# Optimization experiments

Hardware: AMD Instinct MI355X
Metric: run time of the kernel (lower is better)

The kernel has to match this reference:

```python
import jax, jax.numpy as jnp
import numpy as np

N_ENTITIES = 500000
N_RELATIONS = 200
EMBED_DIM = 128
RELATION_DIM = 128  # must equal EMBED_DIM for the reshape in calculate_score
BATCH = 16384
KG_L2_LAMBDA = 1e-5


def _xavier_uniform(key, shape):
    fan_in, fan_out = shape[0], shape[1]
    limit = float(np.sqrt(6.0 / (fan_in + fan_out)))
    return jax.random.uniform(key, shape, jnp.float32, -limit, limit)


def setup_inputs() -> dict:
    key = jax.random.key(0)
    k1, k2, k3, k4, k5, k6 = jax.random.split(key, 6)
    entity_embed = _xavier_uniform(k1, (N_ENTITIES, EMBED_DIM))
    relation_embed = _xavier_uniform(k2, (N_RELATIONS, RELATION_DIM * EMBED_DIM))
    h = jax.random.randint(k3, (BATCH,), 0, N_ENTITIES, dtype=jnp.int64)
    r = jax.random.randint(k4, (BATCH,), 0, N_RELATIONS, dtype=jnp.int64)
    pos_t = jax.random.randint(k5, (BATCH,), 0, N_ENTITIES, dtype=jnp.int64)
    neg_t = jax.random.randint(k6, (BATCH,), 0, N_ENTITIES, dtype=jnp.int64)
    return {"h": h, "r": r, "pos_t": pos_t, "neg_t": neg_t,
            "entity_embed": entity_embed, "relation_embed": relation_embed}


def _l2_loss_mean(x):
    # mean over batch of sum(x^2, dim=1) / 2
    return jnp.mean(jnp.sum(x * x, axis=1) / 2.0)


def _score(h_e, t_e, r_mat):
    # r_mat: (B, relation_dim, embed_dim); tr = r @ t : (B, embed_dim)
    tr = jnp.einsum('bde,be->bd', r_mat, t_e)
    return -jnp.sum(h_e * tr, axis=-1)  # (B,)


def reference(h, r, pos_t, neg_t, entity_embed, relation_embed):
    r_embed = relation_embed[r]                     # (B, R*D)
    head_embed = entity_embed[h]                    # (B, D)
    tail_pos_embed = entity_embed[pos_t]            # (B, D)
    tail_neg_embed = entity_embed[neg_t]            # (B, D)
    r_mat = r_embed.reshape(-1, RELATION_DIM, EMBED_DIM)
    pos_score = _score(head_embed, tail_pos_embed, r_mat)
    neg_score = _score(head_embed, tail_neg_embed, r_mat)
    triplet_loss = jnp.mean(-jax.nn.log_sigmoid(neg_score - pos_score))
    l2_loss = (_l2_loss_mean(head_embed) + _l2_loss_mean(r_embed)
               + _l2_loss_mean(tail_pos_embed) + _l2_loss_mean(tail_neg_embed))
    return triplet_loss + KG_L2_LAMBDA * l2_loss
```

## Files before the change

kernel.cpp:

```cpp
#include <hip/hip_runtime.h>
#include <math.h>

#define BATCH 16384
#define EDIM 128
#define RD (EDIM * EDIM)
#define NREL 200
#define SPLIT 4
#define NBLK (NREL * SPLIT)
#define NTHR 512
#define QUARTER (BATCH / SPLIT)
#define NJ (QUARTER / NTHR)
#define EBW 4
#define LISTCAP 256


__device__ __forceinline__ int load_idx(const void* p, int b, int is64) {
    if (is64) return (int)((const long long*)p)[b];
    return ((const int*)p)[b];
}

__global__ __launch_bounds__(NTHR, 4) void rescal_kernel(
    const void* __restrict__ hI, const void* __restrict__ rI,
    const void* __restrict__ pI, const void* __restrict__ nI,
    const float* __restrict__ ent, const float* __restrict__ rel,
    float* __restrict__ csum) {
    const int t = threadIdx.x;
    const int bid0 = blockIdx.x;
    const int xcd = bid0 & 7;
    const int slot = bid0 >> 3;
    const int rid = xcd + 8 * (slot >> 2);
    const int qtr = slot & 3;
    const int lane = t & 63;
    const int wave = t >> 6;
    const int c2 = lane * 2;

    __shared__ __attribute__((aligned(16))) float Rl[RD];
    __shared__ unsigned short list[LISTCAP];
    __shared__ unsigned int wtj[NJ][8];
    __shared__ unsigned int um8[8];
    __shared__ float rsq[8], wsum[8];

    unsigned int o = 0u;
    if (t < 256) {
        o = ((const unsigned int*)hI)[2 * t + 1] | ((const unsigned int*)rI)[2 * t + 1] |
            ((const unsigned int*)pI)[2 * t + 1] | ((const unsigned int*)nI)[2 * t + 1];
    }
#pragma unroll
    for (int off = 32; off; off >>= 1) o |= __shfl_xor(o, off, 64);
    if (lane == 0) um8[wave] = o;
    __syncthreads();
    const int is64 = ((um8[0] | um8[1] | um8[2] | um8[3] |
                       um8[4] | um8[5] | um8[6] | um8[7]) == 0u) ? 1 : 0;

    const float* Rg = rel + (size_t)rid * RD;
    float r2p = 0.f;
#pragma unroll
    for (int it = 0; it < 8; ++it) {
        const int idx = it * (NTHR * 4) + t * 4;
        const float4 v = *(const float4*)(Rg + idx);
        *(float4*)&Rl[idx] = v;
        r2p = fmaf(v.x, v.x, fmaf(v.y, v.y, fmaf(v.z, v.z, fmaf(v.w, v.w, r2p))));
    }
#pragma unroll
    for (int off = 32; off; off >>= 1) r2p += __shfl_xor(r2p, off, 64);
    if (lane == 0) rsq[wave] = r2p;

    const int qbase = qtr * QUARTER;
    unsigned long long bal[NJ];
#pragma unroll
    for (int j = 0; j < NJ; ++j) {
        const int rr = load_idx(rI, qbase + j * NTHR + t, is64);
        bal[j] = __ballot(rr == rid);
        if (lane == 0) wtj[j][wave] = (unsigned int)__popcll(bal[j]);
    }
    __syncthreads();

    int cnt;
    {
        unsigned int run = 0;
        const unsigned long long ltmask = (lane == 63) ? ~0ull >> 1
                                                       : (1ull << lane) - 1ull;
#pragma unroll
        for (int j = 0; j < NJ; ++j) {
            unsigned int wpre = 0, tj = 0;
#pragma unroll
            for (int w = 0; w < 8; ++w) {
                const unsigned int v = wtj[j][w];
                tj += v;
                wpre += (w < wave) ? v : 0;
            }
            if ((bal[j] >> lane) & 1ull) {
                const unsigned int rank =
                    run + wpre + (unsigned int)__popcll(bal[j] & ltmask);
                if (rank < LISTCAP) list[rank] = (unsigned short)(j * NTHR + t);
            }
            run += tj;
        }
        cnt = (int)run;
        if (cnt > LISTCAP) cnt = LISTCAP;
    }
    __syncthreads();

    const float r2sum = rsq[0] + rsq[1] + rsq[2] + rsq[3] +
                        rsq[4] + rsq[5] + rsq[6] + rsq[7];

    const int per_wave = (cnt + 7) >> 3;
    int lo = wave * per_wave;
    int hi = (wave + 1) * per_wave;
    if (lo > cnt) lo = cnt;
    if (hi > cnt) hi = cnt;

    float lsum = 0.f;

    for (int e0 = lo; e0 < hi; e0 += EBW) {
        int bidx[EBW];
        const float* hrow[EBW];
#pragma unroll
        for (int i = 0; i < EBW; ++i) {
            int e = e0 + i;
            if (e >= hi) e = hi - 1;
            int b = qbase + (int)list[e];
            b = __builtin_amdgcn_readfirstlane(b);
            bidx[i] = b;
            int hix = load_idx(hI, b, is64);
            hix = __builtin_amdgcn_readfirstlane(hix);
            hrow[i] = ent + (size_t)hix * EDIM;
        }

        float2 acc[EBW];
#pragma unroll
        for (int i = 0; i < EBW; ++i) acc[i] = make_float2(0.f, 0.f);
#pragma unroll 4
        for (int db = 0; db < 32; ++db) {
            const float4 hv0 = *(const float4*)(hrow[0] + db * 4);
            const float4 hv1 = *(const float4*)(hrow[1] + db * 4);
            const float4 hv2 = *(const float4*)(hrow[2] + db * 4);
            const float4 hv3 = *(const float4*)(hrow[3] + db * 4);
#pragma unroll
            for (int jj = 0; jj < 4; ++jj) {
                const int d = db * 4 + jj;
                const float2 rv = *(const float2*)&Rl[d * EDIM + c2];
                const float h0 = (jj == 0) ? hv0.x : (jj == 1) ? hv0.y : (jj == 2) ? hv0.z : hv0.w;
                const float h1 = (jj == 0) ? hv1.x : (jj == 1) ? hv1.y : (jj == 2) ? hv1.z : hv1.w;
                const float h2 = (jj == 0) ? hv2.x : (jj == 1) ? hv2.y : (jj == 2) ? hv2.z : hv2.w;
                const float h3 = (jj == 0) ? hv3.x : (jj == 1) ? hv3.y : (jj == 2) ? hv3.z : hv3.w;
                acc[0].x = fmaf(rv.x, h0, acc[0].x); acc[0].y = fmaf(rv.y, h0, acc[0].y);
                acc[1].x = fmaf(rv.x, h1, acc[1].x); acc[1].y = fmaf(rv.y, h1, acc[1].y);
                acc[2].x = fmaf(rv.x, h2, acc[2].x); acc[2].y = fmaf(rv.y, h2, acc[2].y);
                acc[3].x = fmaf(rv.x, h3, acc[3].x); acc[3].y = fmaf(rv.y, h3, acc[3].y);
            }
        }

#pragma unroll
        for (int i = 0; i < EBW; ++i) {
            const int b = bidx[i];
            const int pi = __builtin_amdgcn_readfirstlane(load_idx(pI, b, is64));
            const int ni = __builtin_amdgcn_readfirstlane(load_idx(nI, b, is64));
            const float2 hv2 = *(const float2*)(hrow[i] + c2);
            const float2 tp2 = *(const float2*)(ent + (size_t)pi * EDIM + c2);
            const float2 tn2 = *(const float2*)(ent + (size_t)ni * EDIM + c2);
            float dp = acc[i].x * tp2.x + acc[i].y * tp2.y;
            float dn = acc[i].x * tn2.x + acc[i].y * tn2.y;
            float e2 = hv2.x * hv2.x + hv2.y * hv2.y + tp2.x * tp2.x + tp2.y * tp2.y +
                       tn2.x * tn2.x + tn2.y * tn2.y;
#pragma unroll
            for (int off = 32; off; off >>= 1) {
                dp += __shfl_xor(dp, off, 64);
                dn += __shfl_xor(dn, off, 64);
                e2 += __shfl_xor(e2, off, 64);
            }
            if (lane == 0 && (e0 + i) < hi) {
                const float x = dn - dp;
                const float spl = (x > 0.f) ? (x + log1pf(expf(-x))) : log1pf(expf(x));
                lsum += spl + 1e-5f * 0.5f * (e2 + r2sum);
            }
        }
    }

    if (lane == 0) wsum[wave] = lsum;
    __syncthreads();
    if (t == 0) {
        csum[bid0] = wsum[0] + wsum[1] + wsum[2] + wsum[3] +
                     wsum[4] + wsum[5] + wsum[6] + wsum[7];
    }
}

__global__ __launch_bounds__(256) void reduce_kernel(const float* __restrict__ csum,
                                                     float* __restrict__ out) {
    const int t = threadIdx.x;
    float a = 0.f;
    for (int i = t; i < NBLK; i += 256) a += csum[i];
#pragma unroll
    for (int off = 32; off; off >>= 1) a += __shfl_down(a, off, 64);
    __shared__ float sm[4];
    if ((t & 63) == 0) sm[t >> 6] = a;
    __syncthreads();
    if (t == 0) out[0] = (sm[0] + sm[1] + sm[2] + sm[3]) * (1.0f / (float)BATCH);
}

extern "C" void kernel_launch(void* const* d_in, const int* in_sizes, int n_in,
                              void* d_out, int out_size, void* d_ws, size_t ws_size,
                              hipStream_t stream) {
    const void* h = d_in[0];
    const void* r = d_in[1];
    const void* pt = d_in[2];
    const void* nt = d_in[3];
    const float* ent = (const float*)d_in[4];
    const float* rel = (const float*)d_in[5];
    float* csum = (float*)d_ws;

    rescal_kernel<<<NBLK, NTHR, 0, stream>>>(h, r, pt, nt, ent, rel, csum);
    reduce_kernel<<<1, 256, 0, stream>>>(csum, (float*)d_out);
}
```

Before: 47.24 us.

## Stage head rows in LDS, prefetch tail rows early, halve relation splits

Each wave now loads its head rows cooperatively, one float2 per lane, and stores them in a per-wave LDS buffer. The inner loop then reads the head values from LDS instead of issuing scalar/global float4 loads per row. The tail rows are loaded before the matvec loop so their latency overlaps with compute. The batch split per relation drops from 4 to 2, which halves the block count and the redundant relation-matrix loads, and the entity batch width goes from 4 to 3. The risks are lower parallelism with 400 blocks, more LDS use per block, and a possible LDS read hazard because there is no wave barrier between writing hL and reading it.

Result: no change. 48.01 us (+1.6%).

```diff
diff --git a/kernel.cpp b/kernel.cpp
--- a/kernel.cpp
+++ b/kernel.cpp
@@ -5,12 +5,12 @@
 #define EDIM 128
 #define RD (EDIM * EDIM)
 #define NREL 200
-#define SPLIT 4
+#define SPLIT 2
 #define NBLK (NREL * SPLIT)
 #define NTHR 512
-#define QUARTER (BATCH / SPLIT)
-#define NJ (QUARTER / NTHR)
-#define EBW 4
+#define HALF (BATCH / SPLIT)
+#define NJ (HALF / NTHR)
+#define EBW 3
 #define LISTCAP 256
 
 
@@ -28,13 +28,14 @@
     const int bid0 = blockIdx.x;
     const int xcd = bid0 & 7;
     const int slot = bid0 >> 3;
-    const int rid = xcd + 8 * (slot >> 2);
-    const int qtr = slot & 3;
+    const int rid = xcd + 8 * (slot >> 1);
+    const int half = slot & 1;
     const int lane = t & 63;
     const int wave = t >> 6;
     const int c2 = lane * 2;
 
     __shared__ __attribute__((aligned(16))) float Rl[RD];
+    __shared__ __attribute__((aligned(16))) float hL[8][EBW][EDIM];
     __shared__ unsigned short list[LISTCAP];
     __shared__ unsigned int wtj[NJ][8];
     __shared__ unsigned int um8[8];
@@ -65,7 +66,7 @@
     for (int off = 32; off; off >>= 1) r2p += __shfl_xor(r2p, off, 64);
     if (lane == 0) rsq[wave] = r2p;
 
-    const int qbase = qtr * QUARTER;
+    const int qbase = half * HALF;
     unsigned long long bal[NJ];
 #pragma unroll
     for (int j = 0; j < NJ; ++j) {
@@ -114,7 +115,7 @@
 
     for (int e0 = lo; e0 < hi; e0 += EBW) {
         int bidx[EBW];
-        const float* hrow[EBW];
+        float2 h2[EBW];
 #pragma unroll
         for (int i = 0; i < EBW; ++i) {
             int e = e0 + i;
@@ -124,7 +125,18 @@
             bidx[i] = b;
             int hix = load_idx(hI, b, is64);
             hix = __builtin_amdgcn_readfirstlane(hix);
-            hrow[i] = ent + (size_t)hix * EDIM;
+            h2[i] = *(const float2*)(ent + (size_t)hix * EDIM + c2);
+            *(float2*)&hL[wave][i][c2] = h2[i];
+        }
+
+        float2 tpv[EBW], tnv[EBW];
+#pragma unroll
+        for (int i = 0; i < EBW; ++i) {
+            const int b = bidx[i];
+            const int pi = __builtin_amdgcn_readfirstlane(load_idx(pI, b, is64));
+            const int ni = __builtin_amdgcn_readfirstlane(load_idx(nI, b, is64));
+            tpv[i] = *(const float2*)(ent + (size_t)pi * EDIM + c2);
+            tnv[i] = *(const float2*)(ent + (size_t)ni * EDIM + c2);
         }
 
         float2 acc[EBW];
@@ -132,37 +144,29 @@
         for (int i = 0; i < EBW; ++i) acc[i] = make_float2(0.f, 0.f);
 #pragma unroll 4
         for (int db = 0; db < 32; ++db) {
-            const float4 hv0 = *(const float4*)(hrow[0] + db * 4);
-            const float4 hv1 = *(const float4*)(hrow[1] + db * 4);
-            const float4 hv2 = *(const float4*)(hrow[2] + db * 4);
-            const float4 hv3 = *(const float4*)(hrow[3] + db * 4);
+            const float4 hv0 = *(const float4*)&hL[wave][0][db * 4];
+            const float4 hv1 = *(const float4*)&hL[wave][1][db * 4];
+            const float4 hv2 = *(const float4*)&hL[wave][2][db * 4];
 #pragma unroll
             for (int jj = 0; jj < 4; ++jj) {
                 const int d = db * 4 + jj;
                 const float2 rv = *(const float2*)&Rl[d * EDIM + c2];
                 const float h0 = (jj == 0) ? hv0.x : (jj == 1) ? hv0.y : (jj == 2) ? hv0.z : hv0.w;
                 const float h1 = (jj == 0) ? hv1.x : (jj == 1) ? hv1.y : (jj == 2) ? hv1.z : hv1.w;
-                const float h2 = (jj == 0) ? hv2.x : (jj == 1) ? hv2.y : (jj == 2) ? hv2.z : hv2.w;
-                const float h3 = (jj == 0) ? hv3.x : (jj == 1) ? hv3.y : (jj == 2) ? hv3.z : hv3.w;
-                acc[0].x = fmaf(rv.x, h0, acc[0].x); acc[0].y = fmaf(rv.y, h0, acc[0].y);
-                acc[1].x = fmaf(rv.x, h1, acc[1].x); acc[1].y = fmaf(rv.y, h1, acc[1].y);
-                acc[2].x = fmaf(rv.x, h2, acc[2].x); acc[2].y = fmaf(rv.y, h2, acc[2].y);
-                acc[3].x = fmaf(rv.x, h3, acc[3].x); acc[3].y = fmaf(rv.y, h3, acc[3].y);
+                const float h2b = (jj == 0) ? hv2.x : (jj == 1) ? hv2.y : (jj == 2) ? hv2.z : hv2.w;
+                acc[0].x = fmaf(rv.x, h0, acc[0].x);  acc[0].y = fmaf(rv.y, h0, acc[0].y);
+                acc[1].x = fmaf(rv.x, h1, acc[1].x);  acc[1].y = fmaf(rv.y, h1, acc[1].y);
+                acc[2].x = fmaf(rv.x, h2b, acc[2].x); acc[2].y = fmaf(rv.y, h2b, acc[2].y);
             }
         }
 
 #pragma unroll
         for (int i = 0; i < EBW; ++i) {
-            const int b = bidx[i];
-            const int pi = __builtin_amdgcn_readfirstlane(load_idx(pI, b, is64));
-            const int ni = __builtin_amdgcn_readfirstlane(load_idx(nI, b, is64));
-            const float2 hv2 = *(const float2*)(hrow[i] + c2);
-            const float2 tp2 = *(const float2*)(ent + (size_t)pi * EDIM + c2);
-            const float2 tn2 = *(const float2*)(ent + (size_t)ni * EDIM + c2);
-            float dp = acc[i].x * tp2.x + acc[i].y * tp2.y;
-            float dn = acc[i].x * tn2.x + acc[i].y * tn2.y;
-            float e2 = hv2.x * hv2.x + hv2.y * hv2.y + tp2.x * tp2.x + tp2.y * tp2.y +
-                       tn2.x * tn2.x + tn2.y * tn2.y;
+            float dp = acc[i].x * tpv[i].x + acc[i].y * tpv[i].y;
+            float dn = acc[i].x * tnv[i].x + acc[i].y * tnv[i].y;
+            float e2 = h2[i].x * h2[i].x + h2[i].y * h2[i].y +
+                       tpv[i].x * tpv[i].x + tpv[i].y * tpv[i].y +
+                       tnv[i].x * tnv[i].x + tnv[i].y * tnv[i].y;
 #pragma unroll
             for (int off = 32; off; off >>= 1) {
                 dp += __shfl_xor(dp, off, 64);
```
